# Kernel tuning notes

Hardware: AMD Instinct MI355X
Metric: run time of the kernel (lower is better)

Reference implementation:

```python
import math
import jax, jax.numpy as jnp
import numpy as np

VMIN, VMAX, NUM_BINS = 0.0, 1.0, 64
BIN_WIDTH = (VMAX - VMIN) / NUM_BINS
SIGMA = BIN_WIDTH * (1.0 / (2.0 * math.sqrt(2.0 * math.log(2.0))))
EPS = 1e-10


def setup_inputs() -> dict:
    key = jax.random.key(0)
    kx, ky = jax.random.split(key)
    shape = (2, 1, 96, 96, 96)
    x = jax.random.uniform(kx, shape, dtype=jnp.float32)
    y = jax.random.uniform(ky, shape, dtype=jnp.float32)
    return {"x": x, "y": y}


def _gauss_win(v, bins):
    # v: (N, P), bins: (B,) -> (N, B, P)
    d = v[:, None, :] - bins[None, :, None]
    # NOTE: faithful to source: exp(.)/sqrt(2*pi) * sigma (multiplies by sigma)
    return jnp.exp(-(d * d) / (2.0 * SIGMA * SIGMA)) / math.sqrt(2.0 * math.pi) * SIGMA


def reference(x, y):
    N = x.shape[0]
    xf = x.reshape(N, -1)  # (N, P); dim=1 channel folded into P
    yf = y.reshape(N, -1)
    bins = jnp.linspace(VMIN, VMAX, NUM_BINS, dtype=x.dtype)
    win_x = _gauss_win(xf, bins)  # (N, B, P)
    win_y = _gauss_win(yf, bins)  # (N, B, P)
    hist_joint = jnp.einsum('nbp,ncp->nbc', win_x, win_y)  # (N, B, B)
    hist_norm = hist_joint.sum(axis=(1, 2)) + EPS
    p_joint = hist_joint / hist_norm[:, None, None]
    p_x = p_joint.sum(axis=2)
    p_y = p_joint.sum(axis=1)
    ent_x = -jnp.sum(p_x * jnp.log(p_x + EPS), axis=1)
    ent_y = -jnp.sum(p_y * jnp.log(p_y + EPS), axis=1)
    ent_joint = -jnp.sum(p_joint * jnp.log(p_joint + EPS), axis=(1, 2))
    # normalised=True branch
    return -jnp.mean((ent_x + ent_y) / ent_joint)
```

## Files before the change

kernel.cpp:

```cpp
#include <hip/hip_runtime.h>
#include <math.h>


#define NBINS 64
#define LDA2 72
#define TILEH (NBINS * LDA2)

typedef _Float16 half8    __attribute__((ext_vector_type(8)));
typedef float    floatx16 __attribute__((ext_vector_type(16)));

static constexpr double kSigmaD = 0.015625 / 2.3548200450309493;
static constexpr double kAcD    = (1.0 / (63.0 * 63.0)) / (2.0 * kSigmaD * kSigmaD);
static constexpr float  kAc     = (float)kAcD;
static constexpr float  kEps    = 1e-10f;

__device__ __forceinline__ float bsum128(float v, volatile float* sm) {
#pragma unroll
    for (int off = 32; off > 0; off >>= 1) v += __shfl_down(v, off, 64);
    __syncthreads();
    if ((threadIdx.x & 63) == 0) sm[threadIdx.x >> 6] = v;
    __syncthreads();
    return sm[0] + sm[1];
}

__global__ __launch_bounds__(128, 2) void hist_gemm_kernel(
        const float* __restrict__ x, const float* __restrict__ y,
        float* __restrict__ hist, int* __restrict__ counter,
        float* __restrict__ out, int P, int elemsPerWave, int totalBlocks) {
    __shared__ __align__(16) _Float16 tiles[2][2][NBINS][LDA2];
    __shared__ float smr[2];
    __shared__ int   sIsLast;

    const int t    = threadIdx.x;
    const int lane = t & 63;
    const int wave = t >> 6;
    const int n    = blockIdx.y;

    _Float16* __restrict__ Ax = &tiles[wave][0][0][0];
    _Float16* __restrict__ By = &tiles[wave][1][0][0];

    {
        float4* p4 = (float4*)Ax;
        const int n16 = 2 * TILEH * 2 / 16;
        for (int i = lane; i < n16; i += 64) p4[i] = float4{0.f, 0.f, 0.f, 0.f};
    }

    floatx16 acc[2][2] = {};
    const float* __restrict__ xp = x + (size_t)n * P;
    const float* __restrict__ yp = y + (size_t)n * P;

    const int waveBase = (blockIdx.x * 2 + wave) * elemsPerWave;
    int lim = P - waveBase;
    if (lim > elemsPerWave) lim = elemsPerWave;
    const int nChunks = (elemsPerWave + 63) / 64;

#define GLOAD(c2, ox, oy) do {                                   \
        int off_ = (c2) * 64 + lane;                             \
        int g_ = waveBase + ((off_ < lim) ? off_ : 0);           \
        g_ = min(g_, P - 1);                                     \
        ox = xp[g_]; oy = yp[g_];                                \
    } while (0)

    int pcx = 2, pcy = 2;
    float vx, vy;
    GLOAD(0, vx, vy);

    for (int c = 0; c < nChunks; ++c) {
        float nvx = 0.f, nvy = 0.f;
        if (c + 1 < nChunks) GLOAD(c + 1, nvx, nvy);

        const bool valid = (c * 64 + lane) < lim;
        float wx[5], wy[5];
        int cx = 2, cy = 2;
        if (valid) {
            const float sx = vx * 63.0f;
            const float sy = vy * 63.0f;
            cx = min(max((int)(sx + 0.5f), 2), 61);
            cy = min(max((int)(sy + 0.5f), 2), 61);
            const float dx = sx - (float)cx;
            const float dy = sy - (float)cy;
#pragma unroll
            for (int k = 0; k < 5; ++k) {
                const float ddx = dx - (float)(k - 2);
                const float ddy = dy - (float)(k - 2);
                wx[k] = __expf(-kAc * ddx * ddx);
                wy[k] = __expf(-kAc * ddy * ddy);
            }
        } else {
#pragma unroll
            for (int k = 0; k < 5; ++k) { wx[k] = 0.0f; wy[k] = 0.0f; }
        }

#pragma unroll
        for (int k = 0; k < 5; ++k) {
            Ax[(pcx - 2 + k) * LDA2 + lane] = (_Float16)0.0f;
            By[(pcy - 2 + k) * LDA2 + lane] = (_Float16)0.0f;
        }
#pragma unroll
        for (int k = 0; k < 5; ++k) {
            Ax[(cx - 2 + k) * LDA2 + lane] = (_Float16)wx[k];
            By[(cy - 2 + k) * LDA2 + lane] = (_Float16)wy[k];
        }
        pcx = cx; pcy = cy;

        const int mrow = lane & 31;
        const int kq   = 8 * (lane >> 5);
        const _Float16* pa = &Ax[mrow * LDA2 + kq];
        const _Float16* pb = &By[mrow * LDA2 + kq];
#pragma unroll
        for (int kb = 0; kb < 4; ++kb) {
            const half8 a0 = *(const half8*)(pa + kb * 16);
            const half8 a1 = *(const half8*)(pa + 32 * LDA2 + kb * 16);
            const half8 b0 = *(const half8*)(pb + kb * 16);
            const half8 b1 = *(const half8*)(pb + 32 * LDA2 + kb * 16);
            acc[0][0] = __builtin_amdgcn_mfma_f32_32x32x16_f16(a0, b0, acc[0][0], 0, 0, 0);
            acc[0][1] = __builtin_amdgcn_mfma_f32_32x32x16_f16(a0, b1, acc[0][1], 0, 0, 0);
            acc[1][0] = __builtin_amdgcn_mfma_f32_32x32x16_f16(a1, b0, acc[1][0], 0, 0, 0);
            acc[1][1] = __builtin_amdgcn_mfma_f32_32x32x16_f16(a1, b1, acc[1][1], 0, 0, 0);
        }

        vx = nvx; vy = nvy;
    }
#undef GLOAD

    float* wsum = (float*)&tiles[wave][0][0][0];
#pragma unroll
    for (int qi = 0; qi < 2; ++qi)
#pragma unroll
        for (int qj = 0; qj < 2; ++qj)
#pragma unroll
            for (int r = 0; r < 16; ++r) {
                const int row = qi * 32 + (r & 3) + 8 * (r >> 2) + 4 * (lane >> 5);
                const int col = qj * 32 + (lane & 31);
                wsum[row * NBINS + col] = acc[qi][qj][r];
            }
    __syncthreads();

    float* __restrict__ gh = hist + (size_t)n * NBINS * NBINS;
    const float* w0 = (const float*)&tiles[0][0][0][0];
    const float* w1 = (const float*)&tiles[1][0][0][0];
    for (int i = t; i < NBINS * NBINS; i += 128) {
        atomicAdd(&gh[i], w0[i] + w1[i]);
    }

    __syncthreads();
    asm volatile("" ::: "memory");
    if (t == 0) {
        asm volatile("s_waitcnt vmcnt(0)" ::: "memory");
        int done = __hip_atomic_fetch_add(counter, 1, __ATOMIC_RELAXED,
                                          __HIP_MEMORY_SCOPE_AGENT);
        sIsLast = (done == totalBlocks - 1);
    }
    __syncthreads();
    if (!sIsLast) return;

    float* hl = (float*)&tiles[0][0][0][0];
    for (int i = t; i < 2 * NBINS * NBINS; i += 128)
        hl[i] = __hip_atomic_load(&hist[i], __ATOMIC_RELAXED,
                                  __HIP_MEMORY_SCOPE_AGENT);
    __syncthreads();

    float res = 0.0f;
    for (int n2 = 0; n2 < 2; ++n2) {
        const float* h = hl + n2 * NBINS * NBINS;

        float s = 0.0f;
        for (int i = t; i < NBINS * NBINS; i += 128) s += h[i];
        const float S = bsum128(s, smr) + kEps;
        const float invS = 1.0f / S;

        float ej = 0.0f;
        for (int i = t; i < NBINS * NBINS; i += 128) {
            const float p = h[i] * invS;
            ej += p * __logf(p + kEps);
        }
        const float EJ = bsum128(ej, smr);

        float m = 0.0f;
        if (t < NBINS) {
            float px = 0.0f;
            const float* rp = &h[t * NBINS];
            for (int c2 = 0; c2 < NBINS; ++c2) px += rp[(c2 + t) & 63];
            px *= invS;
            m = px * __logf(px + kEps);
        } else {
            const int c2 = t - NBINS;
            float py = 0.0f;
            for (int b = 0; b < NBINS; ++b) py += h[b * NBINS + c2];
            py *= invS;
            m = py * __logf(py + kEps);
        }
        const float EXY = bsum128(m, smr);
        res += EXY / EJ;
    }
    if (t == 0) out[0] = -0.5f * res;
}

extern "C" void kernel_launch(void* const* d_in, const int* in_sizes, int n_in,
                              void* d_out, int out_size, void* d_ws, size_t ws_size,
                              hipStream_t stream) {
    const float* x = (const float*)d_in[0];
    const float* y = (const float*)d_in[1];
    float* hist    = (float*)d_ws;
    int*   counter = (int*)((char*)d_ws + 2 * NBINS * NBINS * sizeof(float));
    float* out     = (float*)d_out;

    const int N = 2;
    const int P = in_sizes[0] / N;
    const int blocksPerN   = 512;
    const int elemsPerWave = P / (blocksPerN * 2);
    const int totalBlocks  = blocksPerN * N;

    hipMemsetAsync(d_ws, 0, 2 * NBINS * NBINS * sizeof(float) + 64, stream);

    dim3 grid(blocksPerN, N);
    hist_gemm_kernel<<<grid, 128, 0, stream>>>(x, y, hist, counter, out,
                                               P, elemsPerWave, totalBlocks);
}
```

Before: 123.2 us.

## Spread histogram atomics across sixteen partial buffers with two-level reduction

Instead of all 1024 blocks atomically adding into one 64x64 histogram per batch, blocks now add into one of 16 partial buffers chosen by block index, with rotated start offsets to spread address contention. The last block per partial group folds its buffer into the final histogram, and the last of those runs the entropy epilogue. This targets atomic serialization on hot addresses, at the cost of a larger memset and an extra reduction stage with added counter synchronization.

Result: slower. 129.2 us (+4.9%).

```diff
diff --git a/kernel.cpp b/kernel.cpp
--- a/kernel.cpp
+++ b/kernel.cpp
@@ -5,6 +5,8 @@
 #define NBINS 64
 #define LDA2 72
 #define TILEH (NBINS * LDA2)
+#define KBUF 16
+#define HSZ  (NBINS * NBINS)
 
 typedef _Float16 half8    __attribute__((ext_vector_type(8)));
 typedef float    floatx16 __attribute__((ext_vector_type(16)));
@@ -25,11 +27,13 @@
 
 __global__ __launch_bounds__(128, 2) void hist_gemm_kernel(
         const float* __restrict__ x, const float* __restrict__ y,
-        float* __restrict__ hist, int* __restrict__ counter,
-        float* __restrict__ out, int P, int elemsPerWave, int totalBlocks) {
+        float* __restrict__ pbuf,
+        float* __restrict__ hist,
+        int*   __restrict__ ctrs,
+        float* __restrict__ out, int P, int elemsPerWave) {
     __shared__ __align__(16) _Float16 tiles[2][2][NBINS][LDA2];
     __shared__ float smr[2];
-    __shared__ int   sIsLast;
+    __shared__ int   sRole;
 
     const int t    = threadIdx.x;
     const int lane = t & 63;
@@ -136,41 +140,65 @@
             }
     __syncthreads();
 
-    float* __restrict__ gh = hist + (size_t)n * NBINS * NBINS;
+    const int kb  = blockIdx.x & (KBUF - 1);
+    const int rot = ((blockIdx.x >> 4) * 128) & (HSZ - 1);
+    float* __restrict__ gp = pbuf + ((size_t)kb * 2 + n) * HSZ;
     const float* w0 = (const float*)&tiles[0][0][0][0];
     const float* w1 = (const float*)&tiles[1][0][0][0];
-    for (int i = t; i < NBINS * NBINS; i += 128) {
-        atomicAdd(&gh[i], w0[i] + w1[i]);
-    }
-
-    __syncthreads();
-    asm volatile("" ::: "memory");
+    for (int s = 0; s < HSZ / 128; ++s) {
+        const int j = (t + s * 128 + rot) & (HSZ - 1);
+        atomicAdd(&gp[j], w0[j] + w1[j]);
+    }
+
+    const int gid = n * KBUF + kb;
+    int* __restrict__ L1 = ctrs + gid * 16;
+    int* __restrict__ L0 = ctrs + 2 * KBUF * 16;
+    __syncthreads();
     if (t == 0) {
         asm volatile("s_waitcnt vmcnt(0)" ::: "memory");
-        int done = __hip_atomic_fetch_add(counter, 1, __ATOMIC_RELAXED,
-                                          __HIP_MEMORY_SCOPE_AGENT);
-        sIsLast = (done == totalBlocks - 1);
-    }
-    __syncthreads();
-    if (!sIsLast) return;
+        int v = __hip_atomic_fetch_add(L1, 1, __ATOMIC_RELAXED,
+                                       __HIP_MEMORY_SCOPE_AGENT);
+        sRole = (v == 31) ? 1 : 0;
+    }
+    __syncthreads();
+    if (sRole == 0) return;
+
+    {
+        float* __restrict__ hn = hist + (size_t)n * HSZ;
+        for (int s = 0; s < HSZ / 128; ++s) {
+            const int j = (t + s * 128 + kb * 256) & (HSZ - 1);
+            const float v = __hip_atomic_load(&gp[j], __ATOMIC_RELAXED,
+                                              __HIP_MEMORY_SCOPE_AGENT);
+            atomicAdd(&hn[j], v);
+        }
+    }
+    __syncthreads();
+    if (t == 0) {
+        asm volatile("s_waitcnt vmcnt(0)" ::: "memory");
+        int v2 = __hip_atomic_fetch_add(L0, 1, __ATOMIC_RELAXED,
+                                        __HIP_MEMORY_SCOPE_AGENT);
+        sRole = (v2 == 2 * KBUF - 1) ? 2 : 0;
+    }
+    __syncthreads();
+    if (sRole != 2) return;
 
     float* hl = (float*)&tiles[0][0][0][0];
-    for (int i = t; i < 2 * NBINS * NBINS; i += 128)
+    for (int i = t; i < 2 * HSZ; i += 128)
         hl[i] = __hip_atomic_load(&hist[i], __ATOMIC_RELAXED,
                                   __HIP_MEMORY_SCOPE_AGENT);
     __syncthreads();
 
     float res = 0.0f;
     for (int n2 = 0; n2 < 2; ++n2) {
-        const float* h = hl + n2 * NBINS * NBINS;
+        const float* h = hl + n2 * HSZ;
 
         float s = 0.0f;
-        for (int i = t; i < NBINS * NBINS; i += 128) s += h[i];
+        for (int i = t; i < HSZ; i += 128) s += h[i];
         const float S = bsum128(s, smr) + kEps;
         const float invS = 1.0f / S;
 
         float ej = 0.0f;
-        for (int i = t; i < NBINS * NBINS; i += 128) {
+        for (int i = t; i < HSZ; i += 128) {
             const float p = h[i] * invS;
             ej += p * __logf(p + kEps);
         }
@@ -201,19 +229,20 @@
                               hipStream_t stream) {
     const float* x = (const float*)d_in[0];
     const float* y = (const float*)d_in[1];
-    float* hist    = (float*)d_ws;
-    int*   counter = (int*)((char*)d_ws + 2 * NBINS * NBINS * sizeof(float));
-    float* out     = (float*)d_out;
+    char*  ws   = (char*)d_ws;
+    float* pbuf = (float*)ws;
+    float* hist = (float*)(ws + 524288);
+    int*   ctrs = (int*)  (ws + 524288 + 32768);
+    float* out  = (float*)d_out;
 
     const int N = 2;
     const int P = in_sizes[0] / N;
     const int blocksPerN   = 512;
     const int elemsPerWave = P / (blocksPerN * 2);
-    const int totalBlocks  = blocksPerN * N;
-
-    hipMemsetAsync(d_ws, 0, 2 * NBINS * NBINS * sizeof(float) + 64, stream);
+
+    hipMemsetAsync(d_ws, 0, 524288 + 32768 + 32 * 64 + 64, stream);
 
     dim3 grid(blocksPerN, N);
-    hist_gemm_kernel<<<grid, 128, 0, stream>>>(x, y, hist, counter, out,
-                                               P, elemsPerWave, totalBlocks);
+    hist_gemm_kernel<<<grid, 128, 0, stream>>>(x, y, pbuf, hist, ctrs, out,
+                                               P, elemsPerWave);
 }
```
